# Performance work log

Measured on AMD Instinct MI355X. Metric: run time of the kernel, lower is better.

Reference implementation:

```python
import jax, jax.numpy as jnp
import numpy as np

B, N, D_IN, D_OUT = 8, 2048, 128, 64
NEG_INF = -9e15
LEAKY_ALPHA = 0.2


def setup_inputs() -> dict:
    key = jax.random.key(0)
    k_h, k_adj, k_w, k_a = jax.random.split(key, 4)
    h = jax.random.normal(k_h, (B, N, D_IN), dtype=jnp.float32)
    # sparse-ish 0/1 adjacency with forced self-loops (diagonal ones)
    adj = (jax.random.uniform(k_adj, (B, N, N)) < 0.02).astype(jnp.float32)
    adj = jnp.maximum(adj, jnp.eye(N, dtype=jnp.float32)[None, :, :])
    # glorot uniform init for w and a
    lim_w = np.sqrt(6.0 / (D_IN + D_OUT))
    w = jax.random.uniform(k_w, (D_IN, D_OUT), minval=-lim_w, maxval=lim_w, dtype=jnp.float32)
    lim_a = np.sqrt(6.0 / (2 * D_OUT + 1))
    a = jax.random.uniform(k_a, (2 * D_OUT, 1), minval=-lim_a, maxval=lim_a, dtype=jnp.float32)
    return {"h": h, "adj": adj, "w": w, "a": a}


def reference(h, adj, w, a):
    # wh: (B, N, D_OUT)
    wh = jnp.einsum('bnd,df->bnf', h, w)
    # Split a into the halves acting on source (i) and target (j) features.
    # concat([wh_i, wh_j]) @ a == wh_i @ a1 + wh_j @ a2  (exact same math,
    # avoids materializing the (B,N,N,2F) pairwise tensor).
    f = wh.shape[-1]
    s1 = wh @ a[:f, 0]   # (B, N) -> score contribution of node i (rows)
    s2 = wh @ a[f:, 0]   # (B, N) -> score contribution of node j (cols)
    scores = s1[:, :, None] + s2[:, None, :]            # (B, N, N)
    scores = jnp.where(scores >= 0, scores, LEAKY_ALPHA * scores)  # LeakyReLU(0.2)
    masked = jnp.where(adj > 0, scores, NEG_INF)
    coeffs = jax.nn.softmax(masked, axis=2)             # (B, N, N)
    new_h = jnp.einsum('bij,bjf->bif', coeffs, wh)      # (B, N, D_OUT)
    return new_h
```

## Files before the change

### kernel.cpp

```cpp
#include <hip/hip_runtime.h>
#include <hip/hip_bf16.h>
#include <math.h>


#define GAT_B 8
#define GAT_N 2048
#define GAT_DIN 128
#define GAT_DOUT 64
#define GAT_CAP 192

__global__ __launch_bounds__(256) void gat_wh_kernel(
    const float* __restrict__ h, const float* __restrict__ w,
    const float* __restrict__ a, float* __restrict__ wh,
    float* __restrict__ s1, float* __restrict__ s2) {
  __shared__ float w_lds[GAT_DIN * GAT_DOUT];
  __shared__ float h_lds[4][GAT_DIN];

  for (int t = threadIdx.x; t < (GAT_DIN * GAT_DOUT) / 4; t += 256)
    ((float4*)w_lds)[t] = ((const float4*)w)[t];

  const int lane = threadIdx.x & 63;
  const int wv = threadIdx.x >> 6;
  const float a1 = a[lane];
  const float a2 = a[GAT_DOUT + lane];

  const int ngroups = (GAT_B * GAT_N) / 4;
  for (int rg = blockIdx.x; rg < ngroups; rg += gridDim.x) {
    __syncthreads();
    const float4* hsrc = (const float4*)(h + (size_t)rg * 4 * GAT_DIN);
    for (int t = threadIdx.x; t < (4 * GAT_DIN) / 4; t += 256)
      ((float4*)&h_lds[0][0])[t] = hsrc[t];
    __syncthreads();

    const int row = rg * 4 + wv;
    float acc = 0.f;
#pragma unroll 16
    for (int d = 0; d < GAT_DIN; ++d)
      acc = fmaf(h_lds[wv][d], w_lds[d * GAT_DOUT + lane], acc);

    wh[(size_t)row * GAT_DOUT + lane] = acc;

    float t1 = acc * a1, t2 = acc * a2;
#pragma unroll
    for (int off = 32; off >= 1; off >>= 1) {
      t1 += __shfl_xor(t1, off);
      t2 += __shfl_xor(t2, off);
    }
    if (lane == 0) { s1[row] = t1; s2[row] = t2; }
  }
}

__global__ __launch_bounds__(256, 4) void gat_row_kernel(
    const float* __restrict__ adj, const float* __restrict__ wh,
    const float* __restrict__ s1, const float* __restrict__ s2,
    float* __restrict__ out) {
  __shared__ float s2_lds[GAT_N];
  __shared__ float sc_l[4][GAT_CAP];
  __shared__ unsigned short idx_l[4][GAT_CAP];

  const int lane = threadIdx.x & 63;
  const int wv = threadIdx.x >> 6;
  const int b = blockIdx.x >> 7;
  const int g = blockIdx.x & 127;
  const int row0 = (b << 11) + g * 16 + wv * 4;

  const float* whb = wh + ((size_t)b << 11) * GAT_DOUT;
  float* my_sc = sc_l[wv];
  unsigned short* my_idx = idx_l[wv];

  float4 avA[8], avB[8];
  {
    const float* ar = adj + (size_t)row0 * GAT_N;
#pragma unroll
    for (int u = 0; u < 8; ++u)
      avA[u] = *(const float4*)(ar + u * 256 + lane * 4);
  }

  {
    const float4* src = (const float4*)(s2 + ((size_t)b << 11));
    float4* dst = (float4*)s2_lds;
    dst[threadIdx.x] = src[threadIdx.x];
    dst[threadIdx.x + 256] = src[threadIdx.x + 256];
  }
  __syncthreads();

#pragma unroll
  for (int i = 0; i < 4; ++i) {
    const float4* av = (i & 1) ? avB : avA;
    if (i < 3) {
      float4* nxt = (i & 1) ? avA : avB;
      const float* ar = adj + (size_t)(row0 + i + 1) * GAT_N;
#pragma unroll
      for (int u = 0; u < 8; ++u)
        nxt[u] = *(const float4*)(ar + u * 256 + lane * 4);
    }

    const int row = row0 + i;
    const float s1i = s1[row];

    int base = 0;
    float cmax = -1e30f;
#pragma unroll
    for (int u = 0; u < 8; ++u) {
#pragma unroll
      for (int comp = 0; comp < 4; ++comp) {
        const float a_c = (comp == 0) ? av[u].x : (comp == 1) ? av[u].y
                         : (comp == 2) ? av[u].z : av[u].w;
        const bool pred = a_c > 0.f;
        const unsigned long long msk = __ballot(pred);
        if (msk) {
          const int prefix = __builtin_amdgcn_mbcnt_hi(
              (unsigned)(msk >> 32),
              __builtin_amdgcn_mbcnt_lo((unsigned)msk, 0u));
          if (pred) {
            const int p = base + prefix;
            if (p < GAT_CAP) {
              const int j = u * 256 + lane * 4 + comp;
              float sc = s1i + s2_lds[j];
              sc = (sc >= 0.f) ? sc : 0.2f * sc;
              my_sc[p] = sc;
              my_idx[p] = (unsigned short)j;
              cmax = fmaxf(cmax, sc);
            }
          }
          base += (int)__popcll(msk);
        }
      }
    }
    base = min(base, GAT_CAP);

#pragma unroll
    for (int off = 32; off >= 1; off >>= 1)
      cmax = fmaxf(cmax, __shfl_xor(cmax, off));
    const float m = cmax;

    float lsum = 0.f;
#pragma unroll
    for (int k = 0; k < 3; ++k) {
      const int t = k * 64 + lane;
      if (t < base) {
        const float e = __expf(my_sc[t] - m);
        my_sc[t] = e;
        lsum += e;
      }
    }
#pragma unroll
    for (int off = 32; off >= 1; off >>= 1)
      lsum += __shfl_xor(lsum, off);
    const float inv = 1.f / lsum;

    float A0 = 0.f, A1 = 0.f, A2 = 0.f, A3 = 0.f;
    int t = 0;
    for (; t + 4 <= base; t += 4) {
      const float w0 = my_sc[t],     w1 = my_sc[t + 1];
      const float w2 = my_sc[t + 2], w3 = my_sc[t + 3];
      const int j0 = my_idx[t],      j1 = my_idx[t + 1];
      const int j2 = my_idx[t + 2],  j3 = my_idx[t + 3];
      A0 = fmaf(w0, whb[(size_t)j0 * GAT_DOUT + lane], A0);
      A1 = fmaf(w1, whb[(size_t)j1 * GAT_DOUT + lane], A1);
      A2 = fmaf(w2, whb[(size_t)j2 * GAT_DOUT + lane], A2);
      A3 = fmaf(w3, whb[(size_t)j3 * GAT_DOUT + lane], A3);
    }
    for (; t < base; ++t) {
      A0 = fmaf(my_sc[t], whb[(size_t)my_idx[t] * GAT_DOUT + lane], A0);
    }

    out[(size_t)row * GAT_DOUT + lane] = ((A0 + A1) + (A2 + A3)) * inv;
  }
}

extern "C" void kernel_launch(void* const* d_in, const int* in_sizes, int n_in,
                              void* d_out, int out_size, void* d_ws, size_t ws_size,
                              hipStream_t stream) {
  const float* h   = (const float*)d_in[0];
  const float* adj = (const float*)d_in[1];
  const float* w   = (const float*)d_in[2];
  const float* a   = (const float*)d_in[3];
  float* out = (float*)d_out;

  const size_t rows = (size_t)GAT_B * GAT_N;
  float* wh = (float*)d_ws;
  float* s1 = wh + rows * GAT_DOUT;
  float* s2 = s1 + rows;

  gat_wh_kernel<<<1024, 256, 0, stream>>>(h, w, a, wh, s1, s2);
  gat_row_kernel<<<1024, 256, 0, stream>>>(adj, wh, s1, s2, out);
}
```

Before: 69.91 us.

## Compress adjacency to bitmask in separate pass, then aggregate one row per wave

```diff
diff --git a/kernel.cpp b/kernel.cpp
--- a/kernel.cpp
+++ b/kernel.cpp
@@ -50,31 +50,43 @@
   }
 }
 
-__global__ __launch_bounds__(256, 4) void gat_row_kernel(
-    const float* __restrict__ adj, const float* __restrict__ wh,
+__global__ __launch_bounds__(256) void gat_bits_kernel(
+    const float* __restrict__ adj, unsigned long long* __restrict__ bm) {
+  const int lane = threadIdx.x & 63;
+  const int wid = blockIdx.x * 4 + (threadIdx.x >> 6);
+#pragma unroll
+  for (int r = 0; r < 2; ++r) {
+    const int row = wid * 2 + r;
+    const float* ar = adj + (size_t)row * GAT_N;
+    unsigned long long* bmrow = bm + (size_t)row * 32;
+#pragma unroll
+    for (int u = 0; u < 8; ++u) {
+      const float4 av = *(const float4*)(ar + u * 256 + lane * 4);
+      const unsigned long long b0 = __ballot(av.x > 0.f);
+      const unsigned long long b1 = __ballot(av.y > 0.f);
+      const unsigned long long b2 = __ballot(av.z > 0.f);
+      const unsigned long long b3 = __ballot(av.w > 0.f);
+      if (lane < 4) {
+        const unsigned long long v = (lane == 0) ? b0 : (lane == 1) ? b1
+                                    : (lane == 2) ? b2 : b3;
+        bmrow[u * 4 + lane] = v;
+      }
+    }
+  }
+}
+
+__global__ __launch_bounds__(256) void gat_agg_kernel(
+    const unsigned int* __restrict__ bm32, const float* __restrict__ wh,
     const float* __restrict__ s1, const float* __restrict__ s2,
     float* __restrict__ out) {
   __shared__ float s2_lds[GAT_N];
-  __shared__ float sc_l[4][GAT_CAP];
-  __shared__ unsigned short idx_l[4][GAT_CAP];
+  __shared__ float2 list_l[4][GAT_CAP];
 
   const int lane = threadIdx.x & 63;
   const int wv = threadIdx.x >> 6;
-  const int b = blockIdx.x >> 7;
-  const int g = blockIdx.x & 127;
-  const int row0 = (b << 11) + g * 16 + wv * 4;
-
-  const float* whb = wh + ((size_t)b << 11) * GAT_DOUT;
-  float* my_sc = sc_l[wv];
-  unsigned short* my_idx = idx_l[wv];
-
-  float4 avA[8], avB[8];
-  {
-    const float* ar = adj + (size_t)row0 * GAT_N;
-#pragma unroll
-    for (int u = 0; u < 8; ++u)
-      avA[u] = *(const float4*)(ar + u * 256 + lane * 4);
-  }
+  const int b = blockIdx.x >> 9;
+  const int g = blockIdx.x & 511;
+  const int row = (b << 11) + g * 4 + wv;
 
   {
     const float4* src = (const float4*)(s2 + ((size_t)b << 11));
@@ -82,91 +94,79 @@
     dst[threadIdx.x] = src[threadIdx.x];
     dst[threadIdx.x + 256] = src[threadIdx.x + 256];
   }
+  const float s1i = s1[row];
+  const float* whb = wh + ((size_t)b << 11) * GAT_DOUT;
   __syncthreads();
 
+  unsigned int mw = bm32[(size_t)row * 64 + lane];
+  const int cnt = __popc(mw);
+
+  int pos = cnt;
 #pragma unroll
-  for (int i = 0; i < 4; ++i) {
-    const float4* av = (i & 1) ? avB : avA;
-    if (i < 3) {
-      float4* nxt = (i & 1) ? avA : avB;
-      const float* ar = adj + (size_t)(row0 + i + 1) * GAT_N;
-#pragma unroll
-      for (int u = 0; u < 8; ++u)
-        nxt[u] = *(const float4*)(ar + u * 256 + lane * 4);
-    }
+  for (int off = 1; off < 64; off <<= 1) {
+    const int v = __shfl_up(pos, off);
+    pos += (lane >= off) ? v : 0;
+  }
+  const int total = __shfl(pos, 63);
+  pos -= cnt;
 
-    const int row = row0 + i;
-    const float s1i = s1[row];
+  const int colbase = (lane >> 3) * 256 + (lane & 1) * 128 + ((lane >> 1) & 3);
 
-    int base = 0;
-    float cmax = -1e30f;
-#pragma unroll
-    for (int u = 0; u < 8; ++u) {
-#pragma unroll
-      for (int comp = 0; comp < 4; ++comp) {
-        const float a_c = (comp == 0) ? av[u].x : (comp == 1) ? av[u].y
-                         : (comp == 2) ? av[u].z : av[u].w;
-        const bool pred = a_c > 0.f;
-        const unsigned long long msk = __ballot(pred);
-        if (msk) {
-          const int prefix = __builtin_amdgcn_mbcnt_hi(
-              (unsigned)(msk >> 32),
-              __builtin_amdgcn_mbcnt_lo((unsigned)msk, 0u));
-          if (pred) {
-            const int p = base + prefix;
-            if (p < GAT_CAP) {
-              const int j = u * 256 + lane * 4 + comp;
-              float sc = s1i + s2_lds[j];
-              sc = (sc >= 0.f) ? sc : 0.2f * sc;
-              my_sc[p] = sc;
-              my_idx[p] = (unsigned short)j;
-              cmax = fmaxf(cmax, sc);
-            }
-          }
-          base += (int)__popcll(msk);
-        }
-      }
-    }
-    base = min(base, GAT_CAP);
+  float lmax = -1e30f;
+  float2* mylist = list_l[wv];
+  int p = pos;
+  while (mw) {
+    const int j = __builtin_ctz(mw);
+    mw &= mw - 1;
+    const int col = colbase + 4 * j;
+    float sc = s1i + s2_lds[col];
+    sc = (sc >= 0.f) ? sc : 0.2f * sc;
+    if (p < GAT_CAP) mylist[p] = make_float2(sc, __uint_as_float((unsigned)col));
+    lmax = fmaxf(lmax, sc);
+    ++p;
+  }
+  const int base = min(total, GAT_CAP);
 
 #pragma unroll
-    for (int off = 32; off >= 1; off >>= 1)
-      cmax = fmaxf(cmax, __shfl_xor(cmax, off));
-    const float m = cmax;
+  for (int off = 32; off >= 1; off >>= 1)
+    lmax = fmaxf(lmax, __shfl_xor(lmax, off));
+  const float m = lmax;
 
-    float lsum = 0.f;
+  float lsum = 0.f;
 #pragma unroll
-    for (int k = 0; k < 3; ++k) {
-      const int t = k * 64 + lane;
-      if (t < base) {
-        const float e = __expf(my_sc[t] - m);
-        my_sc[t] = e;
-        lsum += e;
-      }
+  for (int k = 0; k < 3; ++k) {
+    const int t = k * 64 + lane;
+    if (t < base) {
+      const float e = __expf(mylist[t].x - m);
+      mylist[t].x = e;
+      lsum += e;
     }
+  }
 #pragma unroll
-    for (int off = 32; off >= 1; off >>= 1)
-      lsum += __shfl_xor(lsum, off);
-    const float inv = 1.f / lsum;
+  for (int off = 32; off >= 1; off >>= 1)
+    lsum += __shfl_xor(lsum, off);
+  const float inv = 1.f / lsum;
 
-    float A0 = 0.f, A1 = 0.f, A2 = 0.f, A3 = 0.f;
-    int t = 0;
-    for (; t + 4 <= base; t += 4) {
-      const float w0 = my_sc[t],     w1 = my_sc[t + 1];
-      const float w2 = my_sc[t + 2], w3 = my_sc[t + 3];
-      const int j0 = my_idx[t],      j1 = my_idx[t + 1];
-      const int j2 = my_idx[t + 2],  j3 = my_idx[t + 3];
-      A0 = fmaf(w0, whb[(size_t)j0 * GAT_DOUT + lane], A0);
-      A1 = fmaf(w1, whb[(size_t)j1 * GAT_DOUT + lane], A1);
-      A2 = fmaf(w2, whb[(size_t)j2 * GAT_DOUT + lane], A2);
-      A3 = fmaf(w3, whb[(size_t)j3 * GAT_DOUT + lane], A3);
-    }
-    for (; t < base; ++t) {
-      A0 = fmaf(my_sc[t], whb[(size_t)my_idx[t] * GAT_DOUT + lane], A0);
-    }
+  float A0 = 0.f, A1 = 0.f, A2 = 0.f, A3 = 0.f;
+  int t = 0;
+  for (; t + 4 <= base; t += 4) {
+    const float2 e0 = mylist[t],     e1 = mylist[t + 1];
+    const float2 e2 = mylist[t + 2], e3 = mylist[t + 3];
+    const int j0 = (int)__float_as_uint(e0.y);
+    const int j1 = (int)__float_as_uint(e1.y);
+    const int j2 = (int)__float_as_uint(e2.y);
+    const int j3 = (int)__float_as_uint(e3.y);
+    A0 = fmaf(e0.x, whb[(size_t)j0 * GAT_DOUT + lane], A0);
+    A1 = fmaf(e1.x, whb[(size_t)j1 * GAT_DOUT + lane], A1);
+    A2 = fmaf(e2.x, whb[(size_t)j2 * GAT_DOUT + lane], A2);
+    A3 = fmaf(e3.x, whb[(size_t)j3 * GAT_DOUT + lane], A3);
+  }
+  for (; t < base; ++t) {
+    const float2 e0 = mylist[t];
+    A0 = fmaf(e0.x, whb[(size_t)(int)__float_as_uint(e0.y) * GAT_DOUT + lane], A0);
+  }
 
-    out[(size_t)row * GAT_DOUT + lane] = ((A0 + A1) + (A2 + A3)) * inv;
-  }
+  out[(size_t)row * GAT_DOUT + lane] = ((A0 + A1) + (A2 + A3)) * inv;
 }
 
 extern "C" void kernel_launch(void* const* d_in, const int* in_sizes, int n_in,
@@ -182,7 +182,10 @@
   float* wh = (float*)d_ws;
   float* s1 = wh + rows * GAT_DOUT;
   float* s2 = s1 + rows;
+  unsigned long long* bm = (unsigned long long*)(s2 + rows);
 
+  gat_bits_kernel<<<2048, 256, 0, stream>>>(adj, bm);
   gat_wh_kernel<<<1024, 256, 0, stream>>>(h, w, a, wh, s1, s2);
-  gat_row_kernel<<<1024, 256, 0, stream>>>(adj, wh, s1, s2, out);
+  gat_agg_kernel<<<GAT_B * (GAT_N / 4), 256, 0, stream>>>(
+      (const unsigned int*)bm, wh, s1, s2, out);
 }
```

New measurement: 62.44 us. -10.7%, faster.
